# Kernel tuning notes

Measured on AMD Instinct MI355X. Metric: run time of the kernel, lower is better.

The kernel has to match this reference:

```python
import math
import jax, jax.numpy as jnp
import numpy as np

B, T, C = 4, 2048, 2048
H, HKV, D = 16, 4, 128
REP = H // HKV
EPS = 1e-6


def setup_inputs() -> dict:
    key = jax.random.key(0)
    ks = jax.random.split(key, 5)
    x = jax.random.normal(ks[0], (B, T, C), dtype=jnp.float32)
    # true RoPE angles: theta=10000
    inv_freq = 1.0 / (10000.0 ** (np.arange(0, D, 2, dtype=np.float32) / D))
    angles = np.arange(T, dtype=np.float32)[:, None] * inv_freq[None, :]  # (T, D//2)
    freqs_cis = jnp.asarray(np.stack([np.cos(angles), np.sin(angles)], axis=-1))  # (T, D//2, 2)
    s = 0.02
    Wq = jax.random.normal(ks[1], (C, H * D), dtype=jnp.float32) * s
    Wk = jax.random.normal(ks[2], (C, HKV * D), dtype=jnp.float32) * s
    Wv = jax.random.normal(ks[3], (C, HKV * D), dtype=jnp.float32) * s
    Wc = jax.random.normal(ks[4], (C, C), dtype=jnp.float32) * s
    return {"x": x, "freqs_cis": freqs_cis, "Wq": Wq, "Wk": Wk, "Wv": Wv, "Wc": Wc}


def _rmsnorm(t):
    # x * rsqrt(mean(x^2) + eps) over last dim, computed in fp32
    ms = jnp.mean(t.astype(jnp.float32) ** 2, axis=-1, keepdims=True)
    return t * jax.lax.rsqrt(ms + EPS).astype(t.dtype)


def _rope(t, cos, sin):
    # t: (B, T, h, D); cos/sin: (1, T, 1, D//2)
    tr = t.astype(jnp.float32).reshape(*t.shape[:-1], D // 2, 2)
    t0, t1 = tr[..., 0], tr[..., 1]
    out = jnp.stack([t0 * cos - t1 * sin, t0 * sin + t1 * cos], axis=-1)
    return out.reshape(t.shape).astype(t.dtype)


def reference(x, freqs_cis, Wq, Wk, Wv, Wc):
    q = (x @ Wq).reshape(B, T, H, D)
    k = (x @ Wk).reshape(B, T, HKV, D)
    v = (x @ Wv).reshape(B, T, HKV, D)
    q = _rmsnorm(q)
    k = _rmsnorm(k)
    cos = freqs_cis[:T, :, 0][None, :, None, :]
    sin = freqs_cis[:T, :, 1][None, :, None, :]
    q = _rope(q, cos, sin)
    k = _rope(k, cos, sin)
    # GQA: group query heads per kv head instead of materializing expanded K/V
    qg = q.reshape(B, T, HKV, REP, D)
    scores = jnp.einsum('bqhrd,bkhd->bhrqk', qg, k) * (1.0 / math.sqrt(D))
    causal = jnp.tril(jnp.ones((T, T), dtype=bool))
    scores = jnp.where(causal[None, None, None, :, :], scores, -jnp.inf)
    att = jax.nn.softmax(scores, axis=-1)
    y = jnp.einsum('bhrqk,bkhd->bqhrd', att, v).reshape(B, T, C)
    return y @ Wc
```

## Files before the change

kernel.cpp:

```cpp
#include <hip/hip_runtime.h>
#include <cstdint>

#define B_ 4
#define T_ 2048
#define C_ 2048
#define H_ 16
#define HKV_ 4
#define D_ 128

typedef unsigned short u16;
typedef __bf16 bf16x8 __attribute__((ext_vector_type(8)));
typedef float f32x4 __attribute__((ext_vector_type(4)));
typedef float f32x16 __attribute__((ext_vector_type(16)));

typedef __attribute__((address_space(1))) const void gvoid;
typedef __attribute__((address_space(3))) void lvoid;

static __device__ __forceinline__ void async_cp16(const u16* g, u16* l) {
  __builtin_amdgcn_global_load_lds((gvoid*)g, (lvoid*)l, 16, 0, 0);
}

static __device__ __forceinline__ u16 f2bf(float f) {
  unsigned int x = __builtin_bit_cast(unsigned int, f);
  x += 0x7fffu + ((x >> 16) & 1u);
  return (u16)(x >> 16);
}
static __device__ __forceinline__ float bf2f(u16 u) {
  unsigned int x = ((unsigned int)u) << 16;
  return __builtin_bit_cast(float, x);
}

__global__ void cast_x_kernel(const float* __restrict__ in, u16* __restrict__ out, int n4) {
  int i = blockIdx.x * blockDim.x + threadIdx.x;
  if (i >= n4) return;
  float4 v = ((const float4*)in)[i];
  ushort4 o;
  o.x = f2bf(v.x); o.y = f2bf(v.y); o.z = f2bf(v.z); o.w = f2bf(v.w);
  ((ushort4*)out)[i] = o;
}

__global__ void wtrans_kernel(const float* __restrict__ W, u16* __restrict__ WT, int K, int N) {
  __shared__ float tile[64][65];
  int n0 = blockIdx.x * 64, k0 = blockIdx.y * 64;
  int tid = threadIdx.x;
#pragma unroll
  for (int i = 0; i < 16; i++) {
    int idx = i * 256 + tid;
    int r = idx >> 6, c = idx & 63;
    tile[r][c] = W[(size_t)(k0 + r) * N + n0 + c];
  }
  __syncthreads();
#pragma unroll
  for (int i = 0; i < 16; i++) {
    int idx = i * 256 + tid;
    int r = idx >> 6, c = idx & 63;
    WT[(size_t)(n0 + r) * K + k0 + c] = f2bf(tile[c][r]);
  }
}

template <bool F32OUT>
__global__ __launch_bounds__(256) void gemm_bt(const u16* __restrict__ A, const u16* __restrict__ BT,
                                               void* __restrict__ Cout, int M, int N, int K) {
  __shared__ __align__(16) u16 As[128 * 64];
  __shared__ __align__(16) u16 Bs[128 * 64];
  int tid = threadIdx.x;
  int w = tid >> 6, lane = tid & 63, quad = lane >> 4, lo = lane & 15;
  int wm = w >> 1, wn = w & 1;
  int m0 = blockIdx.y * 128, n0 = blockIdx.x * 128;
  int srow = w * 32 + (lane >> 3);
  int schunk = lane & 7;
  int gchunk = schunk ^ (lane >> 3);
  f32x4 acc[4][4] = {};
  for (int k0 = 0; k0 < K; k0 += 64) {
#pragma unroll
    for (int c = 0; c < 4; c++) {
      int r = srow + c * 8;
      async_cp16(&A[(size_t)(m0 + r) * K + k0 + gchunk * 8], &As[r * 64 + schunk * 8]);
      async_cp16(&BT[(size_t)(n0 + r) * K + k0 + gchunk * 8], &Bs[r * 64 + schunk * 8]);
    }
    __syncthreads();
#pragma unroll
    for (int kk = 0; kk < 2; kk++) {
      bf16x8 af[4], bfr[4];
#pragma unroll
      for (int mt = 0; mt < 4; mt++) {
        int r = wm * 64 + mt * 16 + lo;
        af[mt] = *(const bf16x8*)(&As[r * 64 + (((kk * 4 + quad) ^ (lo & 7)) << 3)]);
      }
#pragma unroll
      for (int nt = 0; nt < 4; nt++) {
        int r = wn * 64 + nt * 16 + lo;
        bfr[nt] = *(const bf16x8*)(&Bs[r * 64 + (((kk * 4 + quad) ^ (lo & 7)) << 3)]);
      }
#pragma unroll
      for (int mt = 0; mt < 4; mt++)
#pragma unroll
        for (int nt = 0; nt < 4; nt++)
          acc[mt][nt] = __builtin_amdgcn_mfma_f32_16x16x32_bf16(af[mt], bfr[nt], acc[mt][nt], 0, 0, 0);
    }
    __syncthreads();
  }
#pragma unroll
  for (int mt = 0; mt < 4; mt++)
#pragma unroll
    for (int nt = 0; nt < 4; nt++)
#pragma unroll
      for (int r = 0; r < 4; r++) {
        int mg = m0 + wm * 64 + mt * 16 + quad * 4 + r;
        int ng = n0 + wn * 64 + nt * 16 + lo;
        float v = acc[mt][nt][r];
        if (F32OUT) ((float*)Cout)[(size_t)mg * N + ng] = v;
        else ((u16*)Cout)[(size_t)mg * N + ng] = f2bf(v);
      }
}

__global__ void rmsrope_kernel(const u16* __restrict__ in, const float* __restrict__ freqs,
                               u16* __restrict__ out, int heads, float outscale) {
  int w = threadIdx.x >> 6, lane = threadIdx.x & 63;
  int row = blockIdx.x * 4 + w;
  int hh = row % heads;
  int rest = row / heads;
  int t = rest % T_;
  int b = rest / T_;
  const u16* ip = in + (size_t)row * D_;
  unsigned pr = *(const unsigned*)(&ip[2 * lane]);
  float t0 = bf2f((u16)(pr & 0xffff)), t1 = bf2f((u16)(pr >> 16));
  float ss = t0 * t0 + t1 * t1;
#pragma unroll
  for (int off = 32; off > 0; off >>= 1) ss += __shfl_xor(ss, off, 64);
  float scale = rsqrtf(ss * (1.0f / 128.0f) + 1e-6f) * outscale;
  float2 cs = ((const float2*)freqs)[t * 64 + lane];
  float a = t0 * scale, c = t1 * scale;
  float o0 = a * cs.x - c * cs.y;
  float o1 = a * cs.y + c * cs.x;
  size_t ob = ((size_t)(b * heads + hh) * T_ + t) * D_ + 2 * lane;
  *(unsigned*)(&out[ob]) = ((unsigned)f2bf(o1) << 16) | (unsigned)f2bf(o0);
}

__global__ void vtrans_kernel(const u16* __restrict__ v, u16* __restrict__ vt) {
  __shared__ u16 tile[64][65];
  int bh = blockIdx.x;
  int b = bh >> 2, h = bh & 3;
  int t0 = blockIdx.y * 64, d0 = blockIdx.z * 64;
  const u16* base = v + ((size_t)b * T_ * HKV_ + h) * D_;
  u16* obase = vt + (size_t)bh * D_ * T_;
  int tid = threadIdx.x;
#pragma unroll
  for (int i = 0; i < 16; i++) {
    int idx = i * 256 + tid, tr = idx >> 6, dc = idx & 63;
    tile[tr][dc] = base[(size_t)(t0 + tr) * (HKV_ * D_) + d0 + dc];
  }
  __syncthreads();
#pragma unroll
  for (int i = 0; i < 16; i++) {
    int idx = i * 256 + tid, dr = idx >> 6, tc = idx & 63;
    obase[(size_t)(d0 + dr) * T_ + t0 + tc] = tile[tc][dr];
  }
}

__global__ __launch_bounds__(256) void flash_kernel(const u16* __restrict__ qb, const u16* __restrict__ kb,
                                                    const u16* __restrict__ vb, u16* __restrict__ yb) {
  __shared__ __align__(16) u16 smem[17408];
  u16* Ks = smem;
  u16* Vs = smem + 8192;
  int bh = blockIdx.x;
  int b = bh >> 4, hq = bh & 15;
  int qt = gridDim.y - 1 - blockIdx.y;
  int tid = threadIdx.x, w = tid >> 6, lane = tid & 63;
  int half = lane >> 5, lq = lane & 31;
  int bhkv = b * HKV_ + (hq >> 2);
  const u16* qbase = qb + ((size_t)bh * T_ + qt * 128) * D_;
  const u16* kbase = kb + (size_t)bhkv * T_ * D_;
  const u16* vbase = vb + (size_t)bhkv * D_ * T_;

  bf16x8 qf[8];
#pragma unroll
  for (int ds = 0; ds < 8; ds++)
    qf[ds] = *(const bf16x8*)(&qbase[(w * 32 + lq) * D_ + ds * 16 + half * 8]);

  f32x16 oacc[4] = {};
  float l_part = 0.f;
  const float L2E = 1.4426950408889634f;
  const float N12 = -17.312340490667562f;

  int kchunk = lane & 15, krow0 = w * 16 + (lane >> 4);
  int vchunk = lane & 7, vrow0 = w * 32 + (lane >> 3);
  int qwave = qt * 128 + w * 32;

  int ktmax = 2 * qt + 1;
  for (int kt = 0; kt <= ktmax; kt++) {
    const u16* ksrc = kbase + (size_t)(kt * 64) * D_;
    const u16* vsrc = vbase + kt * 64;
#pragma unroll
    for (int c = 0; c < 4; c++) {
      int r = krow0 + c * 4;
      async_cp16(&ksrc[r * D_ + ((kchunk ^ (r & 7)) << 3)], &Ks[r * 128 + (kchunk << 3)]);
    }
#pragma unroll
    for (int c = 0; c < 4; c++) {
      int r = vrow0 + c * 8;
      async_cp16(&vsrc[(size_t)r * T_ + ((vchunk ^ (r & 7)) << 3)], &Vs[r * 64 + (vchunk << 3)]);
    }
    __syncthreads();

#pragma unroll
    for (int t = 0; t < 2; t++) {
      int k0 = kt * 64 + t * 32;
      if (k0 > qwave + 31) continue;

      f32x16 s = {};
#pragma unroll
      for (int ds = 0; ds < 8; ds++) {
        bf16x8 kf = *(const bf16x8*)(&Ks[(t * 32 + lq) * 128 + ((((ds << 1) + half) ^ (lq & 7)) << 3)]);
        s = __builtin_amdgcn_mfma_f32_32x32x16_bf16(kf, qf[ds], s, 0, 0, 0);
      }

      int qglob = qwave + lq;
      if (k0 + 31 > qwave) {
#pragma unroll
        for (int i = 0; i < 16; i++) {
          int kl = k0 + 4 * half + (i & 3) + ((i >> 2) << 3);
          if (kl > qglob) s[i] = -1e30f;
        }
      }

      unsigned pd[8];
#pragma unroll
      for (int j = 0; j < 8; j++) {
        float p0 = __builtin_amdgcn_exp2f(fmaf(s[2 * j], L2E, N12));
        float p1 = __builtin_amdgcn_exp2f(fmaf(s[2 * j + 1], L2E, N12));
        l_part += p0 + p1;
        pd[j] = ((unsigned)f2bf(p0)) | (((unsigned)f2bf(p1)) << 16);
      }

      unsigned s0 = (unsigned)__shfl_xor((int)(half ? pd[0] : pd[2]), 32, 64);
      unsigned s1 = (unsigned)__shfl_xor((int)(half ? pd[1] : pd[3]), 32, 64);
      unsigned s2 = (unsigned)__shfl_xor((int)(half ? pd[4] : pd[6]), 32, 64);
      unsigned s3 = (unsigned)__shfl_xor((int)(half ? pd[5] : pd[7]), 32, 64);
      uint4 f0 = half ? uint4{s0, s1, pd[2], pd[3]} : uint4{pd[0], pd[1], s0, s1};
      uint4 f1 = half ? uint4{s2, s3, pd[6], pd[7]} : uint4{pd[4], pd[5], s2, s3};

#pragma unroll
      for (int kstep = 0; kstep < 2; kstep++) {
        uint4 fr = kstep ? f1 : f0;
        bf16x8 pf = __builtin_bit_cast(bf16x8, fr);
        int cR = (t * 2 + kstep) * 2 + half;
#pragma unroll
        for (int dt = 0; dt < 4; dt++) {
          bf16x8 vf = *(const bf16x8*)(&Vs[(dt * 32 + lq) * 64 + ((cR ^ (lq & 7)) << 3)]);
          oacc[dt] = __builtin_amdgcn_mfma_f32_32x32x16_bf16(vf, pf, oacc[dt], 0, 0, 0);
        }
      }
    }
    __syncthreads();
  }

  float lt = l_part + __shfl_xor(l_part, 32, 64);
  float inv = 1.0f / lt;

  u16* Ep = smem;
#pragma unroll
  for (int dt = 0; dt < 4; dt++)
#pragma unroll
    for (int j = 0; j < 8; j++) {
      float p0 = oacc[dt][2 * j] * inv;
      float p1 = oacc[dt][2 * j + 1] * inv;
      unsigned pk = ((unsigned)f2bf(p0)) | (((unsigned)f2bf(p1)) << 16);
      int d = dt * 32 + 4 * half + 2 * (j & 1) + ((j >> 1) << 3);
      *(unsigned*)(&Ep[(w * 32 + lq) * 136 + d]) = pk;
    }
  __syncthreads();

  int ic = tid & 15, qr0 = tid >> 4;
  size_t orow = ((size_t)b * T_ + qt * 128) * 2048 + hq * 128;
#pragma unroll
  for (int j = 0; j < 8; j++) {
    int qr = qr0 + j * 16;
    uint4 v4 = *(const uint4*)(&Ep[qr * 136 + ic * 8]);
    *(uint4*)(&yb[orow + (size_t)qr * 2048 + ic * 8]) = v4;
  }
}

extern "C" void kernel_launch(void* const* d_in, const int* in_sizes, int n_in,
                              void* d_out, int out_size, void* d_ws, size_t ws_size,
                              hipStream_t stream) {
  const float* x = (const float*)d_in[0];
  const float* freqs = (const float*)d_in[1];
  const float* Wq = (const float*)d_in[2];
  const float* Wk = (const float*)d_in[3];
  const float* Wv = (const float*)d_in[4];
  const float* Wc = (const float*)d_in[5];
  float* out = (float*)d_out;

  char* ws = (char*)d_ws;
  size_t off = 0;
  auto alloc = [&](size_t bytes) { char* p = ws + off; off += (bytes + 255) & ~255ull; return p; };
  u16* xb  = (u16*)alloc((size_t)B_ * T_ * C_ * 2);
  u16* WqT = (u16*)alloc((size_t)C_ * H_ * D_ * 2);
  u16* WkT = (u16*)alloc((size_t)C_ * HKV_ * D_ * 2);
  u16* WvT = (u16*)alloc((size_t)C_ * HKV_ * D_ * 2);
  u16* WcT = (u16*)alloc((size_t)C_ * C_ * 2);
  u16* qp  = (u16*)alloc((size_t)B_ * T_ * H_ * D_ * 2);
  u16* kp  = (u16*)alloc((size_t)B_ * T_ * HKV_ * D_ * 2);
  u16* vp  = (u16*)alloc((size_t)B_ * T_ * HKV_ * D_ * 2);
  u16* qb  = (u16*)alloc((size_t)B_ * H_ * T_ * D_ * 2);
  u16* kb  = (u16*)alloc((size_t)B_ * HKV_ * T_ * D_ * 2);
  u16* vb  = (u16*)alloc((size_t)B_ * HKV_ * T_ * D_ * 2);
  u16* yb  = (u16*)alloc((size_t)B_ * T_ * H_ * D_ * 2);

  cast_x_kernel<<<dim3(B_ * T_ * C_ / 1024), dim3(256), 0, stream>>>(x, xb, B_ * T_ * C_ / 4);
  wtrans_kernel<<<dim3(32, 32), dim3(256), 0, stream>>>(Wq, WqT, C_, H_ * D_);
  wtrans_kernel<<<dim3(8, 32), dim3(256), 0, stream>>>(Wk, WkT, C_, HKV_ * D_);
  wtrans_kernel<<<dim3(8, 32), dim3(256), 0, stream>>>(Wv, WvT, C_, HKV_ * D_);
  wtrans_kernel<<<dim3(32, 32), dim3(256), 0, stream>>>(Wc, WcT, C_, C_);

  gemm_bt<false><<<dim3(16, 64), dim3(256), 0, stream>>>(xb, WqT, (void*)qp, 8192, 2048, 2048);
  gemm_bt<false><<<dim3(4, 64), dim3(256), 0, stream>>>(xb, WkT, (void*)kp, 8192, 512, 2048);
  gemm_bt<false><<<dim3(4, 64), dim3(256), 0, stream>>>(xb, WvT, (void*)vp, 8192, 512, 2048);

  const float sc = 0.08838834764831845f;
  rmsrope_kernel<<<dim3(B_ * T_ * H_ / 4), dim3(256), 0, stream>>>(qp, freqs, qb, H_, sc);
  rmsrope_kernel<<<dim3(B_ * T_ * HKV_ / 4), dim3(256), 0, stream>>>(kp, freqs, kb, HKV_, 1.0f);
  vtrans_kernel<<<dim3(16, 32, 2), dim3(256), 0, stream>>>(vp, vb);

  flash_kernel<<<dim3(B_ * H_, T_ / 128), dim3(256), 0, stream>>>(qb, kb, vb, yb);

  gemm_bt<true><<<dim3(16, 64), dim3(256), 0, stream>>>(yb, WcT, (void*)out, 8192, 2048, 2048);
}
```

Measured before the change: 541.4 us.

## Fuse QKV projections into one GEMM and pair causal query tiles in flash

Concatenates transposed Wq/Wk/Wv into one weight so a single N=3072 GEMM produces Q, K and V. All weight transposes are merged into one launch, and downstream kernels read from the strided fused buffer. The flash kernel now processes query tiles qt and 15-qt in the same block, so every block does equal causal work and the grid is halved. Probability packing switches to byte-perm truncation instead of rounding, which slightly changes numerics.

```diff
diff --git a/kernel.cpp b/kernel.cpp
--- a/kernel.cpp
+++ b/kernel.cpp
@@ -39,22 +39,31 @@
   ((ushort4*)out)[i] = o;
 }
 
-__global__ void wtrans_kernel(const float* __restrict__ W, u16* __restrict__ WT, int K, int N) {
+__global__ void wtrans_all_kernel(const float* __restrict__ Wq, const float* __restrict__ Wk,
+                                  const float* __restrict__ Wv, const float* __restrict__ Wc,
+                                  u16* __restrict__ Wcat, u16* __restrict__ WcT) {
   __shared__ float tile[64][65];
-  int n0 = blockIdx.x * 64, k0 = blockIdx.y * 64;
+  int tb = blockIdx.x;
+  const float* W; u16* WT; int Nw, t;
+  if (tb < 1024)      { W = Wq; WT = Wcat;                         Nw = 2048; t = tb; }
+  else if (tb < 1280) { W = Wk; WT = Wcat + (size_t)2048 * 2048;   Nw = 512;  t = tb - 1024; }
+  else if (tb < 1536) { W = Wv; WT = Wcat + (size_t)2560 * 2048;   Nw = 512;  t = tb - 1280; }
+  else                { W = Wc; WT = WcT;                          Nw = 2048; t = tb - 1536; }
+  int ntiles = Nw >> 6;
+  int n0 = (t % ntiles) * 64, k0 = (t / ntiles) * 64;
   int tid = threadIdx.x;
 #pragma unroll
   for (int i = 0; i < 16; i++) {
     int idx = i * 256 + tid;
     int r = idx >> 6, c = idx & 63;
-    tile[r][c] = W[(size_t)(k0 + r) * N + n0 + c];
+    tile[r][c] = W[(size_t)(k0 + r) * Nw + n0 + c];
   }
   __syncthreads();
 #pragma unroll
   for (int i = 0; i < 16; i++) {
     int idx = i * 256 + tid;
     int r = idx >> 6, c = idx & 63;
-    WT[(size_t)(n0 + r) * K + k0 + c] = f2bf(tile[c][r]);
+    WT[(size_t)(n0 + r) * 2048 + k0 + c] = f2bf(tile[c][r]);
   }
 }
 
@@ -115,14 +124,14 @@
 }
 
 __global__ void rmsrope_kernel(const u16* __restrict__ in, const float* __restrict__ freqs,
-                               u16* __restrict__ out, int heads, float outscale) {
+                               u16* __restrict__ out, int heads, int instride, float outscale) {
   int w = threadIdx.x >> 6, lane = threadIdx.x & 63;
   int row = blockIdx.x * 4 + w;
   int hh = row % heads;
   int rest = row / heads;
   int t = rest % T_;
   int b = rest / T_;
-  const u16* ip = in + (size_t)row * D_;
+  const u16* ip = in + (size_t)(b * T_ + t) * instride + hh * D_;
   unsigned pr = *(const unsigned*)(&ip[2 * lane]);
   float t0 = bf2f((u16)(pr & 0xffff)), t1 = bf2f((u16)(pr >> 16));
   float ss = t0 * t0 + t1 * t1;
@@ -142,13 +151,13 @@
   int bh = blockIdx.x;
   int b = bh >> 2, h = bh & 3;
   int t0 = blockIdx.y * 64, d0 = blockIdx.z * 64;
-  const u16* base = v + ((size_t)b * T_ * HKV_ + h) * D_;
+  const u16* base = v + (size_t)b * T_ * 3072 + h * D_;
   u16* obase = vt + (size_t)bh * D_ * T_;
   int tid = threadIdx.x;
 #pragma unroll
   for (int i = 0; i < 16; i++) {
     int idx = i * 256 + tid, tr = idx >> 6, dc = idx & 63;
-    tile[tr][dc] = base[(size_t)(t0 + tr) * (HKV_ * D_) + d0 + dc];
+    tile[tr][dc] = base[(size_t)(t0 + tr) * 3072 + d0 + dc];
   }
   __syncthreads();
 #pragma unroll
@@ -165,119 +174,125 @@
   u16* Vs = smem + 8192;
   int bh = blockIdx.x;
   int b = bh >> 4, hq = bh & 15;
-  int qt = gridDim.y - 1 - blockIdx.y;
+  int jp = blockIdx.y;
   int tid = threadIdx.x, w = tid >> 6, lane = tid & 63;
   int half = lane >> 5, lq = lane & 31;
   int bhkv = b * HKV_ + (hq >> 2);
-  const u16* qbase = qb + ((size_t)bh * T_ + qt * 128) * D_;
   const u16* kbase = kb + (size_t)bhkv * T_ * D_;
   const u16* vbase = vb + (size_t)bhkv * D_ * T_;
-
-  bf16x8 qf[8];
-#pragma unroll
-  for (int ds = 0; ds < 8; ds++)
-    qf[ds] = *(const bf16x8*)(&qbase[(w * 32 + lq) * D_ + ds * 16 + half * 8]);
-
-  f32x16 oacc[4] = {};
-  float l_part = 0.f;
   const float L2E = 1.4426950408889634f;
   const float N12 = -17.312340490667562f;
 
   int kchunk = lane & 15, krow0 = w * 16 + (lane >> 4);
   int vchunk = lane & 7, vrow0 = w * 32 + (lane >> 3);
-  int qwave = qt * 128 + w * 32;
-
-  int ktmax = 2 * qt + 1;
-  for (int kt = 0; kt <= ktmax; kt++) {
-    const u16* ksrc = kbase + (size_t)(kt * 64) * D_;
-    const u16* vsrc = vbase + kt * 64;
-#pragma unroll
-    for (int c = 0; c < 4; c++) {
-      int r = krow0 + c * 4;
-      async_cp16(&ksrc[r * D_ + ((kchunk ^ (r & 7)) << 3)], &Ks[r * 128 + (kchunk << 3)]);
+
+  for (int ph = 0; ph < 2; ph++) {
+    int qt = ph ? jp : (15 - jp);
+    const u16* qbase = qb + ((size_t)bh * T_ + qt * 128) * D_;
+    int qwave = qt * 128 + w * 32;
+
+    bf16x8 qf[8];
+#pragma unroll
+    for (int ds = 0; ds < 8; ds++)
+      qf[ds] = *(const bf16x8*)(&qbase[(w * 32 + lq) * D_ + ds * 16 + half * 8]);
+
+    f32x16 oacc[4] = {};
+    float l_part = 0.f;
+
+    int ktmax = 2 * qt + 1;
+    for (int kt = 0; kt <= ktmax; kt++) {
+      const u16* ksrc = kbase + (size_t)(kt * 64) * D_;
+      const u16* vsrc = vbase + kt * 64;
+#pragma unroll
+      for (int c = 0; c < 4; c++) {
+        int r = krow0 + c * 4;
+        async_cp16(&ksrc[r * D_ + ((kchunk ^ (r & 7)) << 3)], &Ks[r * 128 + (kchunk << 3)]);
+      }
+#pragma unroll
+      for (int c = 0; c < 4; c++) {
+        int r = vrow0 + c * 8;
+        async_cp16(&vsrc[(size_t)r * T_ + ((vchunk ^ (r & 7)) << 3)], &Vs[r * 64 + (vchunk << 3)]);
+      }
+      __syncthreads();
+
+#pragma unroll
+      for (int t = 0; t < 2; t++) {
+        int k0 = kt * 64 + t * 32;
+        if (k0 > qwave + 31) continue;
+
+        f32x16 s = {};
+#pragma unroll
+        for (int ds = 0; ds < 8; ds++) {
+          bf16x8 kf = *(const bf16x8*)(&Ks[(t * 32 + lq) * 128 + ((((ds << 1) + half) ^ (lq & 7)) << 3)]);
+          s = __builtin_amdgcn_mfma_f32_32x32x16_bf16(kf, qf[ds], s, 0, 0, 0);
+        }
+
+        int qglob = qwave + lq;
+        if (k0 + 31 > qwave) {
+#pragma unroll
+          for (int i = 0; i < 16; i++) {
+            int kl = k0 + 4 * half + (i & 3) + ((i >> 2) << 3);
+            if (kl > qglob) s[i] = -1e30f;
+          }
+        }
+
+        unsigned pd[8];
+#pragma unroll
+        for (int j2 = 0; j2 < 8; j2++) {
+          float p0 = __builtin_amdgcn_exp2f(fmaf(s[2 * j2], L2E, N12));
+          float p1 = __builtin_amdgcn_exp2f(fmaf(s[2 * j2 + 1], L2E, N12));
+          l_part += p0 + p1;
+          pd[j2] = __builtin_amdgcn_perm(__builtin_bit_cast(unsigned, p1),
+                                         __builtin_bit_cast(unsigned, p0), 0x07060302u);
+        }
+
+        unsigned s0 = (unsigned)__shfl_xor((int)(half ? pd[0] : pd[2]), 32, 64);
+        unsigned s1 = (unsigned)__shfl_xor((int)(half ? pd[1] : pd[3]), 32, 64);
+        unsigned s2 = (unsigned)__shfl_xor((int)(half ? pd[4] : pd[6]), 32, 64);
+        unsigned s3 = (unsigned)__shfl_xor((int)(half ? pd[5] : pd[7]), 32, 64);
+        uint4 f0 = half ? uint4{s0, s1, pd[2], pd[3]} : uint4{pd[0], pd[1], s0, s1};
+        uint4 f1 = half ? uint4{s2, s3, pd[6], pd[7]} : uint4{pd[4], pd[5], s2, s3};
+
+#pragma unroll
+        for (int kstep = 0; kstep < 2; kstep++) {
+          uint4 fr = kstep ? f1 : f0;
+          bf16x8 pf = __builtin_bit_cast(bf16x8, fr);
+          int cR = (t * 2 + kstep) * 2 + half;
+#pragma unroll
+          for (int dt = 0; dt < 4; dt++) {
+            bf16x8 vf = *(const bf16x8*)(&Vs[(dt * 32 + lq) * 64 + ((cR ^ (lq & 7)) << 3)]);
+            oacc[dt] = __builtin_amdgcn_mfma_f32_32x32x16_bf16(vf, pf, oacc[dt], 0, 0, 0);
+          }
+        }
+      }
+      __syncthreads();
     }
-#pragma unroll
-    for (int c = 0; c < 4; c++) {
-      int r = vrow0 + c * 8;
-      async_cp16(&vsrc[(size_t)r * T_ + ((vchunk ^ (r & 7)) << 3)], &Vs[r * 64 + (vchunk << 3)]);
+
+    float lt = l_part + __shfl_xor(l_part, 32, 64);
+    float inv = 1.0f / lt;
+
+    u16* Ep = smem;
+#pragma unroll
+    for (int dt = 0; dt < 4; dt++)
+#pragma unroll
+      for (int j2 = 0; j2 < 8; j2++) {
+        float p0 = oacc[dt][2 * j2] * inv;
+        float p1 = oacc[dt][2 * j2 + 1] * inv;
+        unsigned pk = ((unsigned)f2bf(p0)) | (((unsigned)f2bf(p1)) << 16);
+        int d = dt * 32 + 4 * half + 2 * (j2 & 1) + ((j2 >> 1) << 3);
+        *(unsigned*)(&Ep[(w * 32 + lq) * 136 + d]) = pk;
+      }
+    __syncthreads();
+
+    int ic = tid & 15, qr0 = tid >> 4;
+    size_t orow = ((size_t)b * T_ + qt * 128) * 2048 + hq * 128;
+#pragma unroll
+    for (int j2 = 0; j2 < 8; j2++) {
+      int qr = qr0 + j2 * 16;
+      uint4 v4 = *(const uint4*)(&Ep[qr * 136 + ic * 8]);
+      *(uint4*)(&yb[orow + (size_t)qr * 2048 + ic * 8]) = v4;
     }
     __syncthreads();
-
-#pragma unroll
-    for (int t = 0; t < 2; t++) {
-      int k0 = kt * 64 + t * 32;
-      if (k0 > qwave + 31) continue;
-
-      f32x16 s = {};
-#pragma unroll
-      for (int ds = 0; ds < 8; ds++) {
-        bf16x8 kf = *(const bf16x8*)(&Ks[(t * 32 + lq) * 128 + ((((ds << 1) + half) ^ (lq & 7)) << 3)]);
-        s = __builtin_amdgcn_mfma_f32_32x32x16_bf16(kf, qf[ds], s, 0, 0, 0);
-      }
-
-      int qglob = qwave + lq;
-      if (k0 + 31 > qwave) {
-#pragma unroll
-        for (int i = 0; i < 16; i++) {
-          int kl = k0 + 4 * half + (i & 3) + ((i >> 2) << 3);
-          if (kl > qglob) s[i] = -1e30f;
-        }
-      }
-
-      unsigned pd[8];
-#pragma unroll
-      for (int j = 0; j < 8; j++) {
-        float p0 = __builtin_amdgcn_exp2f(fmaf(s[2 * j], L2E, N12));
-        float p1 = __builtin_amdgcn_exp2f(fmaf(s[2 * j + 1], L2E, N12));
-        l_part += p0 + p1;
-        pd[j] = ((unsigned)f2bf(p0)) | (((unsigned)f2bf(p1)) << 16);
-      }
-
-      unsigned s0 = (unsigned)__shfl_xor((int)(half ? pd[0] : pd[2]), 32, 64);
-      unsigned s1 = (unsigned)__shfl_xor((int)(half ? pd[1] : pd[3]), 32, 64);
-      unsigned s2 = (unsigned)__shfl_xor((int)(half ? pd[4] : pd[6]), 32, 64);
-      unsigned s3 = (unsigned)__shfl_xor((int)(half ? pd[5] : pd[7]), 32, 64);
-      uint4 f0 = half ? uint4{s0, s1, pd[2], pd[3]} : uint4{pd[0], pd[1], s0, s1};
-      uint4 f1 = half ? uint4{s2, s3, pd[6], pd[7]} : uint4{pd[4], pd[5], s2, s3};
-
-#pragma unroll
-      for (int kstep = 0; kstep < 2; kstep++) {
-        uint4 fr = kstep ? f1 : f0;
-        bf16x8 pf = __builtin_bit_cast(bf16x8, fr);
-        int cR = (t * 2 + kstep) * 2 + half;
-#pragma unroll
-        for (int dt = 0; dt < 4; dt++) {
-          bf16x8 vf = *(const bf16x8*)(&Vs[(dt * 32 + lq) * 64 + ((cR ^ (lq & 7)) << 3)]);
-          oacc[dt] = __builtin_amdgcn_mfma_f32_32x32x16_bf16(vf, pf, oacc[dt], 0, 0, 0);
-        }
-      }
-    }
-    __syncthreads();
-  }
-
-  float lt = l_part + __shfl_xor(l_part, 32, 64);
-  float inv = 1.0f / lt;
-
-  u16* Ep = smem;
-#pragma unroll
-  for (int dt = 0; dt < 4; dt++)
-#pragma unroll
-    for (int j = 0; j < 8; j++) {
-      float p0 = oacc[dt][2 * j] * inv;
-      float p1 = oacc[dt][2 * j + 1] * inv;
-      unsigned pk = ((unsigned)f2bf(p0)) | (((unsigned)f2bf(p1)) << 16);
-      int d = dt * 32 + 4 * half + 2 * (j & 1) + ((j >> 1) << 3);
-      *(unsigned*)(&Ep[(w * 32 + lq) * 136 + d]) = pk;
-    }
-  __syncthreads();
-
-  int ic = tid & 15, qr0 = tid >> 4;
-  size_t orow = ((size_t)b * T_ + qt * 128) * 2048 + hq * 128;
-#pragma unroll
-  for (int j = 0; j < 8; j++) {
-    int qr = qr0 + j * 16;
-    uint4 v4 = *(const uint4*)(&Ep[qr * 136 + ic * 8]);
-    *(uint4*)(&yb[orow + (size_t)qr * 2048 + ic * 8]) = v4;
   }
 }
 
@@ -295,35 +310,26 @@
   char* ws = (char*)d_ws;
   size_t off = 0;
   auto alloc = [&](size_t bytes) { char* p = ws + off; off += (bytes + 255) & ~255ull; return p; };
-  u16* xb  = (u16*)alloc((size_t)B_ * T_ * C_ * 2);
-  u16* WqT = (u16*)alloc((size_t)C_ * H_ * D_ * 2);
-  u16* WkT = (u16*)alloc((size_t)C_ * HKV_ * D_ * 2);
-  u16* WvT = (u16*)alloc((size_t)C_ * HKV_ * D_ * 2);
-  u16* WcT = (u16*)alloc((size_t)C_ * C_ * 2);
-  u16* qp  = (u16*)alloc((size_t)B_ * T_ * H_ * D_ * 2);
-  u16* kp  = (u16*)alloc((size_t)B_ * T_ * HKV_ * D_ * 2);
-  u16* vp  = (u16*)alloc((size_t)B_ * T_ * HKV_ * D_ * 2);
-  u16* qb  = (u16*)alloc((size_t)B_ * H_ * T_ * D_ * 2);
-  u16* kb  = (u16*)alloc((size_t)B_ * HKV_ * T_ * D_ * 2);
-  u16* vb  = (u16*)alloc((size_t)B_ * HKV_ * T_ * D_ * 2);
-  u16* yb  = (u16*)alloc((size_t)B_ * T_ * H_ * D_ * 2);
+  u16* xb   = (u16*)alloc((size_t)B_ * T_ * C_ * 2);
+  u16* Wcat = (u16*)alloc((size_t)C_ * 3072 * 2);
+  u16* WcT  = (u16*)alloc((size_t)C_ * C_ * 2);
+  u16* qkvp = (u16*)alloc((size_t)B_ * T_ * 3072 * 2);
+  u16* qb   = (u16*)alloc((size_t)B_ * H_ * T_ * D_ * 2);
+  u16* kb   = (u16*)alloc((size_t)B_ * HKV_ * T_ * D_ * 2);
+  u16* vb   = (u16*)alloc((size_t)B_ * HKV_ * T_ * D_ * 2);
+  u16* yb   = (u16*)alloc((size_t)B_ * T_ * H_ * D_ * 2);
 
   cast_x_kernel<<<dim3(B_ * T_ * C_ / 1024), dim3(256), 0, stream>>>(x, xb, B_ * T_ * C_ / 4);
-  wtrans_kernel<<<dim3(32, 32), dim3(256), 0, stream>>>(Wq, WqT, C_, H_ * D_);
-  wtrans_kernel<<<dim3(8, 32), dim3(256), 0, stream>>>(Wk, WkT, C_, HKV_ * D_);
-  wtrans_kernel<<<dim3(8, 32), dim3(256), 0, stream>>>(Wv, WvT, C_, HKV_ * D_);
-  wtrans_kernel<<<dim3(32, 32), dim3(256), 0, stream>>>(Wc, WcT, C_, C_);
-
-  gemm_bt<false><<<dim3(16, 64), dim3(256), 0, stream>>>(xb, WqT, (void*)qp, 8192, 2048, 2048);
-  gemm_bt<false><<<dim3(4, 64), dim3(256), 0, stream>>>(xb, WkT, (void*)kp, 8192, 512, 2048);
-  gemm_bt<false><<<dim3(4, 64), dim3(256), 0, stream>>>(xb, WvT, (void*)vp, 8192, 512, 2048);
+  wtrans_all_kernel<<<dim3(2560), dim3(256), 0, stream>>>(Wq, Wk, Wv, Wc, Wcat, WcT);
+
+  gemm_bt<false><<<dim3(24, 64), dim3(256), 0, stream>>>(xb, Wcat, (void*)qkvp, 8192, 3072, 2048);
 
   const float sc = 0.08838834764831845f;
-  rmsrope_kernel<<<dim3(B_ * T_ * H_ / 4), dim3(256), 0, stream>>>(qp, freqs, qb, H_, sc);
-  rmsrope_kernel<<<dim3(B_ * T_ * HKV_ / 4), dim3(256), 0, stream>>>(kp, freqs, kb, HKV_, 1.0f);
-  vtrans_kernel<<<dim3(16, 32, 2), dim3(256), 0, stream>>>(vp, vb);
-
-  flash_kernel<<<dim3(B_ * H_, T_ / 128), dim3(256), 0, stream>>>(qb, kb, vb, yb);
+  rmsrope_kernel<<<dim3(B_ * T_ * H_ / 4), dim3(256), 0, stream>>>(qkvp, freqs, qb, H_, 3072, sc);
+  rmsrope_kernel<<<dim3(B_ * T_ * HKV_ / 4), dim3(256), 0, stream>>>(qkvp + 2048, freqs, kb, HKV_, 3072, 1.0f);
+  vtrans_kernel<<<dim3(16, 32, 2), dim3(256), 0, stream>>>(qkvp + 2560, vb);
+
+  flash_kernel<<<dim3(B_ * H_, 8), dim3(256), 0, stream>>>(qb, kb, vb, yb);
 
   gemm_bt<true><<<dim3(16, 64), dim3(256), 0, stream>>>(yb, WcT, (void*)out, 8192, 2048, 2048);
 }
```

After: 478.9 us. 1.13x faster.
